# Kernel tuning notes

Hardware: AMD Instinct MI355X
Metric: run time of the kernel (lower is better)

The kernel has to match this reference:

```python
import jax, jax.numpy as jnp
import numpy as np

B, SI, ST, C, H, D = 1, 1024, 256, 3072, 24, 128
MLP = 4 * C
EPS = 1e-6
SCALE = 1.0 / float(np.sqrt(D))


def _ln(x):
    m = jnp.mean(x, -1, keepdims=True)
    v = jnp.var(x, -1, keepdims=True)
    return (x - m) / jnp.sqrt(v + EPS)


def _rms(x, w):
    return x * jax.lax.rsqrt(jnp.mean(x * x, -1, keepdims=True) + EPS) * w


def _mod(x, shift, scale):
    # AdaLN modulation: x * (1 + scale) + shift, scale/shift are [B, C]
    return x * (1.0 + scale[:, None, :]) + shift[:, None, :]


def _rot_half(x):
    xr, xi = x[..., 0::2], x[..., 1::2]
    return jnp.stack([-xi, xr], -1).reshape(x.shape)


def _rope(x, cos, sin):
    # x: [B, S, H, D]; cos/sin: [S, D]
    return x * cos[None, :, None, :] + _rot_half(x) * sin[None, :, None, :]


def _forward(img, txt, vec, fc, fs,
             i_mod_w, i_mod_b, i_qkv_w, i_qkv_b, i_qn, i_kn, i_pw, i_pb, i_f1w, i_f1b, i_f2w, i_f2b,
             t_mod_w, t_mod_b, t_qkv_w, t_qkv_b, t_qn, t_kn, t_pw, t_pb, t_f1w, t_f1b, t_f2w, t_f2b):
    sv = jax.nn.silu(vec)
    i_s1, i_c1, i_g1, i_s2, i_c2, i_g2 = jnp.split(sv @ i_mod_w + i_mod_b, 6, -1)
    t_s1, t_c1, t_g1, t_s2, t_c2, t_g2 = jnp.split(sv @ t_mod_w + t_mod_b, 6, -1)

    # img stream: LN -> modulate -> QKV -> qk RMSNorm -> RoPE
    iqkv = (_mod(_ln(img), i_s1, i_c1) @ i_qkv_w + i_qkv_b).reshape(B, SI, 3, H, D)
    iq = _rope(_rms(iqkv[:, :, 0], i_qn), fc, fs)
    ik = _rope(_rms(iqkv[:, :, 1], i_kn), fc, fs)
    iv = iqkv[:, :, 2]

    # txt stream: no RoPE
    tqkv = (_mod(_ln(txt), t_s1, t_c1) @ t_qkv_w + t_qkv_b).reshape(B, ST, 3, H, D)
    tq = _rms(tqkv[:, :, 0], t_qn)
    tk = _rms(tqkv[:, :, 1], t_kn)
    tv = tqkv[:, :, 2]

    q = jnp.concatenate([iq, tq], 1)
    k = jnp.concatenate([ik, tk], 1)
    v = jnp.concatenate([iv, tv], 1)

    logits = jnp.einsum('bqhd,bkhd->bhqk', q, k) * SCALE
    o = jnp.einsum('bhqk,bkhd->bqhd', jax.nn.softmax(logits, -1), v).reshape(B, SI + ST, C)
    ia, ta = o[:, :SI], o[:, SI:]

    img = img + (ia @ i_pw + i_pb) * i_g1[:, None, :]
    h = jax.nn.gelu(_mod(_ln(img), i_s2, i_c2) @ i_f1w + i_f1b, approximate=True)
    img = img + (h @ i_f2w + i_f2b) * i_g2[:, None, :]

    txt = txt + (ta @ t_pw + t_pb) * t_g1[:, None, :]
    h = jax.nn.gelu(_mod(_ln(txt), t_s2, t_c2) @ t_f1w + t_f1b, approximate=True)
    txt = txt + (h @ t_f2w + t_f2b) * t_g2[:, None, :]
    return img, txt


def setup_inputs() -> dict:
    key = jax.random.key(0)
    ki = iter(jax.random.split(key, 32))

    def w(shape, s=0.02):
        return jax.random.normal(next(ki), shape, jnp.float32) * s

    # RoPE tables shaped (img_seq_len, head_dim), interleaved pair layout
    pos = jnp.arange(SI, dtype=jnp.float32)
    inv = 1.0 / (10000.0 ** (jnp.arange(0, D, 2, dtype=jnp.float32) / D))
    ang = pos[:, None] * inv[None, :]
    inp = dict(
        img=jax.random.normal(next(ki), (B, SI, C), jnp.float32),
        txt=jax.random.normal(next(ki), (B, ST, C), jnp.float32),
        vec=jax.random.normal(next(ki), (B, C), jnp.float32),
        freqs_cos=jnp.repeat(jnp.cos(ang), 2, -1),
        freqs_sin=jnp.repeat(jnp.sin(ang), 2, -1),
    )
    for p in ('i', 't'):
        inp[p + '_mod_w'] = w((C, 6 * C)); inp[p + '_mod_b'] = jnp.zeros((6 * C,), jnp.float32)
        inp[p + '_qkv_w'] = w((C, 3 * C)); inp[p + '_qkv_b'] = jnp.zeros((3 * C,), jnp.float32)
        inp[p + '_qn'] = jnp.ones((D,), jnp.float32); inp[p + '_kn'] = jnp.ones((D,), jnp.float32)
        inp[p + '_pw'] = w((C, C)); inp[p + '_pb'] = jnp.zeros((C,), jnp.float32)
        inp[p + '_f1w'] = w((C, MLP)); inp[p + '_f1b'] = jnp.zeros((MLP,), jnp.float32)
        inp[p + '_f2w'] = w((MLP, C)); inp[p + '_f2b'] = jnp.zeros((C,), jnp.float32)
    return inp


def reference(img, txt, vec, freqs_cos, freqs_sin,
              i_mod_w, i_mod_b, i_qkv_w, i_qkv_b, i_qn, i_kn, i_pw, i_pb, i_f1w, i_f1b, i_f2w, i_f2b,
              t_mod_w, t_mod_b, t_qkv_w, t_qkv_b, t_qn, t_kn, t_pw, t_pb, t_f1w, t_f1b, t_f2w, t_f2b):
    return _forward(img, txt, vec, freqs_cos, freqs_sin,
                    i_mod_w, i_mod_b, i_qkv_w, i_qkv_b, i_qn, i_kn, i_pw, i_pb, i_f1w, i_f1b, i_f2w, i_f2b,
                    t_mod_w, t_mod_b, t_qkv_w, t_qkv_b, t_qn, t_kn, t_pw, t_pb, t_f1w, t_f1b, t_f2w, t_f2b)
```

## Files before the change

kernel.cpp:

```cpp
#include <hip/hip_runtime.h>


#define SI 1024
#define ST 256
#define SS 1280
#define CC 3072
#define NH 24
#define DH 128
#define MLPD 12288
#define EPSF 1e-6f
#define SCALEF 0.08838834764831845f

typedef __attribute__((ext_vector_type(4))) float f32x4;
typedef __attribute__((ext_vector_type(8))) __bf16 bf16x8;
typedef unsigned short u16;
typedef unsigned int u32;

__device__ __forceinline__ u16 f2bf(float x) {
    union { float f; u32 u; } v; v.f = x;
    u32 r = v.u + 0x7FFFu + ((v.u >> 16) & 1u);
    return (u16)(r >> 16);
}

__device__ __forceinline__ int gsw(int r) {
    return ((r >> 2) & 7) ^ ((r & 3) << 1);
}

__global__ __launch_bounds__(256) void k_modvec(
    const float* __restrict__ vec,
    const float* __restrict__ wi, const float* __restrict__ bi,
    const float* __restrict__ wt, const float* __restrict__ bt,
    float* __restrict__ mi, float* __restrict__ mt)
{
    __shared__ float sv[CC];
    __shared__ float part[7][128];
    int t = threadIdx.x;
    for (int i = t; i < CC; i += 256) {
        float x = vec[i];
        sv[i] = x / (1.f + __expf(-x));
    }
    __syncthreads();
    int gc = blockIdx.x;
    int strm = gc >= 144;
    const float* W  = strm ? wt : wi;
    const float* Bv = strm ? bt : bi;
    float* out      = strm ? mt : mi;
    int c0 = (gc % 144) * 128 + 4 * (t & 31);
    int g  = t >> 5;
    const float* wp  = W + (size_t)(g * 384) * (6 * CC) + c0;
    const float* svp = sv + g * 384;
    f32x4 acc = {0.f, 0.f, 0.f, 0.f};
    for (int r = 0; r < 384; ++r) {
        f32x4 wr = *(const f32x4*)(wp + (size_t)r * (6 * CC));
        float s = svp[r];
        acc.x += wr.x * s; acc.y += wr.y * s; acc.z += wr.z * s; acc.w += wr.w * s;
    }
    int li = t & 31;
    if (g > 0) *(f32x4*)&part[g - 1][li * 4] = acc;
    __syncthreads();
    if (g == 0) {
#pragma unroll
        for (int i = 0; i < 7; ++i) {
            f32x4 p = *(const f32x4*)&part[i][li * 4];
            acc.x += p.x; acc.y += p.y; acc.z += p.z; acc.w += p.w;
        }
        f32x4 bb = *(const f32x4*)(Bv + c0);
        acc.x += bb.x; acc.y += bb.y; acc.z += bb.z; acc.w += bb.w;
        *(f32x4*)(out + c0) = acc;
    }
}

__global__ __launch_bounds__(256) void k_lnmod(
    const float* __restrict__ x,
    const float* __restrict__ shift, const float* __restrict__ scale,
    u16* __restrict__ out)
{
    int r = blockIdx.x;
    const float* xp = x + (size_t)r * CC;
    u16* op = out + (size_t)r * CC;
    int t = threadIdx.x;
    float4 v[3];
    float s = 0.f, q = 0.f;
#pragma unroll
    for (int j = 0; j < 3; ++j) {
        v[j] = *(const float4*)(xp + j * 1024 + t * 4);
        s += v[j].x + v[j].y + v[j].z + v[j].w;
        q += v[j].x * v[j].x + v[j].y * v[j].y + v[j].z * v[j].z + v[j].w * v[j].w;
    }
#pragma unroll
    for (int m = 32; m; m >>= 1) { s += __shfl_xor(s, m); q += __shfl_xor(q, m); }
    __shared__ float red[8];
    int w = t >> 6;
    if ((t & 63) == 0) { red[w] = s; red[4 + w] = q; }
    __syncthreads();
    s = red[0] + red[1] + red[2] + red[3];
    q = red[4] + red[5] + red[6] + red[7];
    float mean = s * (1.f / CC);
    float var  = q * (1.f / CC) - mean * mean;
    float inv  = rsqrtf(var + EPSF);
#pragma unroll
    for (int j = 0; j < 3; ++j) {
        int c0 = j * 1024 + t * 4;
        float4 sh = *(const float4*)(shift + c0);
        float4 sc = *(const float4*)(scale + c0);
        ushort4 o;
        o.x = f2bf((v[j].x - mean) * inv * (1.f + sc.x) + sh.x);
        o.y = f2bf((v[j].y - mean) * inv * (1.f + sc.y) + sh.y);
        o.z = f2bf((v[j].z - mean) * inv * (1.f + sc.z) + sh.z);
        o.w = f2bf((v[j].w - mean) * inv * (1.f + sc.w) + sh.w);
        *(ushort4*)(op + c0) = o;
    }
}

template <int V, int BN>
__global__ __launch_bounds__(512, 2) void k_gemm(
    const u16* __restrict__ A,
    const float* __restrict__ Wi, const float* __restrict__ Wt,
    const float* __restrict__ bi, const float* __restrict__ bt,
    void* __restrict__ outv, int MBI, int N, int K, int lda)
{
    constexpr int BM  = 256;
    constexpr int NWN = (BN == 256) ? 4 : 2;
    constexpr int WM  = (BN == 256) ? 128 : 64;
    constexpr int MI  = WM / 16;
    constexpr int NFB = (BN == 256) ? 8 : 4;

    __shared__ u16 lA[2][BM * 64];
    __shared__ u16 lB[2][BN * 64];
    int t = threadIdx.x;
    int m0 = blockIdx.y * BM;
    int n0 = blockIdx.x * BN;
    bool txts = (blockIdx.y >= (unsigned)MBI);
    const float* W = txts ? Wt : Wi;
    const size_t koff = (size_t)blockIdx.z * K;

    int w = t >> 6, lane = t & 63;
    int wm = (w / NWN) * WM, wn = (w % NWN) * 64;
    int lr = lane & 15, lg = lane >> 4;

    f32x4 acc[MI][4];
#pragma unroll
    for (int i = 0; i < MI; ++i)
#pragma unroll
        for (int j = 0; j < 4; ++j) acc[i][j] = (f32x4){0.f, 0.f, 0.f, 0.f};

    const int bn4 = (BN == 256) ? 4 * (t & 63) : 4 * (t & 31);
    const int bk  = (BN == 256) ? 8 * (t >> 6) : 4 * (t >> 5);
    f32x4 fb[NFB];
    const int NT = K >> 6;

    auto LOADB = [&](int kt) {
        size_t kb = koff + (size_t)kt * 64 + bk;
#pragma unroll
        for (int i = 0; i < NFB; ++i)
            fb[i] = *(const f32x4*)(W + (kb + i) * (size_t)N + n0 + bn4);
    };
    auto GLDSA = [&](int kt, int buf) {
        size_t kb = koff + (size_t)kt * 64;
#pragma unroll
        for (int i = 0; i < 4; ++i) {
            int D = i * 512 + t; int row = D >> 3;
            int c = (D & 7) ^ gsw(row);
            const u16* gp = A + (size_t)(m0 + row) * lda + kb + c * 8;
            u16* lp = &lA[buf][D * 8];
            __builtin_amdgcn_global_load_lds(
                (const __attribute__((address_space(1))) void*)gp,
                (__attribute__((address_space(3))) void*)lp, 16, 0, 0);
        }
    };
    auto CVTWR = [&](int buf) {
        if constexpr (BN == 256) {
#pragma unroll
            for (int j = 0; j < 4; ++j) {
                int n = bn4 + j;
                union { uint4 q; __bf16 h[8]; } u;
#pragma unroll
                for (int i = 0; i < 8; ++i) u.h[i] = (__bf16)fb[i][j];
                int cp = (bk >> 3) ^ gsw(n);
                *(uint4*)&lB[buf][n * 64 + cp * 8] = u.q;
            }
        } else {
#pragma unroll
            for (int j = 0; j < 4; ++j) {
                int n = bn4 + j;
                union { uint2 q; __bf16 h[4]; } u;
#pragma unroll
                for (int i = 0; i < 4; ++i) u.h[i] = (__bf16)fb[i][j];
                int cp = (bk >> 3) ^ gsw(n);
                *(uint2*)&lB[buf][n * 64 + cp * 8 + (bk & 4)] = u.q;
            }
        }
    };
    auto MFMAP = [&](int buf) {
#pragma unroll
        for (int ks = 0; ks < 2; ++ks) {
            bf16x8 bv[4];
#pragma unroll
            for (int j = 0; j < 4; ++j) {
                int n = wn + j * 16 + lr;
                bv[j] = *(const bf16x8*)&lB[buf][n * 64 + (((ks * 4 + lg) ^ gsw(n)) * 8)];
            }
#pragma unroll
            for (int mh = 0; mh < MI / 4; ++mh) {
                bf16x8 af[4];
#pragma unroll
                for (int i2 = 0; i2 < 4; ++i2) {
                    int m = wm + (mh * 4 + i2) * 16 + lr;
                    af[i2] = *(const bf16x8*)&lA[buf][m * 64 + (((ks * 4 + lg) ^ gsw(m)) * 8)];
                }
                __builtin_amdgcn_s_setprio(1);
#pragma unroll
                for (int i2 = 0; i2 < 4; ++i2)
#pragma unroll
                    for (int j = 0; j < 4; ++j)
                        acc[mh * 4 + i2][j] = __builtin_amdgcn_mfma_f32_16x16x32_bf16(
                            af[i2], bv[j], acc[mh * 4 + i2][j], 0, 0, 0);
                __builtin_amdgcn_s_setprio(0);
            }
        }
    };
    auto VMWN = [&]() {
        if constexpr (BN == 256)
            asm volatile("s_waitcnt vmcnt(8) lgkmcnt(0)" ::: "memory");
        else
            asm volatile("s_waitcnt vmcnt(4) lgkmcnt(0)" ::: "memory");
    };

    LOADB(0);
    GLDSA(0, 0);
    CVTWR(0);
    if (NT > 1) LOADB(1);
    VMWN();
    __builtin_amdgcn_s_barrier();
    __builtin_amdgcn_sched_barrier(0);

    int cur = 0;
    for (int kt = 0; kt < NT; ++kt) {
        bool s1 = kt + 1 < NT;
        bool s2 = kt + 2 < NT;
        if (s1) {
            GLDSA(kt + 1, cur ^ 1);
            CVTWR(cur ^ 1);
        }
        if (s2) LOADB(kt + 2);
        MFMAP(cur);
        if (s1) {
            if (s2) { VMWN(); }
            else    { asm volatile("s_waitcnt vmcnt(0) lgkmcnt(0)" ::: "memory"); }
            __builtin_amdgcn_s_barrier();
            __builtin_amdgcn_sched_barrier(0);
        }
        cur ^= 1;
    }

    const float* Bb = txts ? bt : bi;
    int MT = gridDim.y * BM;
#pragma unroll
    for (int i = 0; i < MI; ++i) {
#pragma unroll
        for (int j = 0; j < 4; ++j) {
            int col = n0 + wn + j * 16 + lr;
            float bvv = (V == 3) ? 0.f : Bb[col];
#pragma unroll
            for (int e = 0; e < 4; ++e) {
                int row = m0 + wm + i * 16 + lg * 4 + e;
                float val = acc[i][j][e] + bvv;
                if (V == 0) {
                    ((float*)outv)[(size_t)row * N + col] = val;
                } else if (V == 1) {
                    float g = 0.5f * val * (1.f + tanhf(0.7978845608028654f * (val + 0.044715f * val * val * val)));
                    ((u16*)outv)[(size_t)row * N + col] = f2bf(g);
                } else {
                    ((float*)outv)[((size_t)blockIdx.z * MT + row) * N + col] = val;
                }
            }
        }
    }
}

__global__ __launch_bounds__(256) void k_red(
    const float* __restrict__ p,
    const float* __restrict__ bi, const float* __restrict__ bt,
    const float* __restrict__ gi, const float* __restrict__ gt,
    const float* __restrict__ basei, const float* __restrict__ baset,
    float* __restrict__ out)
{
    int idx4 = blockIdx.x * 256 + threadIdx.x;
    size_t idx = (size_t)idx4 * 4;
    const size_t MN = (size_t)SS * CC;
    int r = idx4 / 768;
    int c = (idx4 - r * 768) * 4;
    bool ts = r >= SI;
    float4 v0 = *(const float4*)(p + idx);
    float4 v1 = *(const float4*)(p + MN + idx);
    float4 bb = *(const float4*)((ts ? bt : bi) + c);
    float4 gg = *(const float4*)((ts ? gt : gi) + c);
    const float* bp = ts ? (baset + (size_t)(r - SI) * CC + c) : (basei + (size_t)r * CC + c);
    float4 ba = *(const float4*)bp;
    float4 o;
    o.x = ba.x + (v0.x + v1.x + bb.x) * gg.x;
    o.y = ba.y + (v0.y + v1.y + bb.y) * gg.y;
    o.z = ba.z + (v0.z + v1.z + bb.z) * gg.z;
    o.w = ba.w + (v0.w + v1.w + bb.w) * gg.w;
    *(float4*)(out + idx) = o;
}

__global__ __launch_bounds__(256) void k_pack(
    const float* __restrict__ qkv,
    const float* __restrict__ iqn, const float* __restrict__ ikn,
    const float* __restrict__ tqn, const float* __restrict__ tkn,
    const float* __restrict__ fc, const float* __restrict__ fs,
    u16* __restrict__ qpk, u16* __restrict__ kpk, u16* __restrict__ vpk)
{
    int wid = blockIdx.x * 4 + (threadIdx.x >> 6);
    int lane = threadIdx.x & 63;
    int s = wid / 72;
    int wh = wid % 72;
    int which = wh / 24;
    int h = wh % 24;
    int d = lane * 2;
    const float* src = qkv + (size_t)s * 9216 + which * 3072 + h * 128 + d;
    float x0 = src[0], x1 = src[1];
    float y0 = x0, y1 = x1;
    if (which < 2) {
        float ssq = x0 * x0 + x1 * x1;
#pragma unroll
        for (int m = 32; m; m >>= 1) ssq += __shfl_xor(ssq, m);
        float inv = rsqrtf(ssq * (1.f / 128.f) + EPSF);
        bool isimg = (s < SI);
        const float* wv = (which == 0) ? (isimg ? iqn : tqn) : (isimg ? ikn : tkn);
        y0 = x0 * inv * wv[d];
        y1 = x1 * inv * wv[d + 1];
        if (isimg) {
            float c0 = fc[s * 128 + d], c1 = fc[s * 128 + d + 1];
            float s0 = fs[s * 128 + d], s1 = fs[s * 128 + d + 1];
            float r0 = y0 * c0 - y1 * s0;
            float r1 = y1 * c1 + y0 * s1;
            y0 = r0; y1 = r1;
        }
        if (which == 0) { y0 *= SCALEF; y1 *= SCALEF; }
    }
    u16* dst = (which == 0) ? qpk : (which == 1) ? kpk : vpk;
    ushort2 o; o.x = f2bf(y0); o.y = f2bf(y1);
    *(ushort2*)(dst + ((size_t)h * SS + s) * 128 + d) = o;
}

__global__ __launch_bounds__(256, 1) void k_attn(
    const u16* __restrict__ qpk, const u16* __restrict__ kpk,
    const u16* __restrict__ vpk, u16* __restrict__ o)
{
    __shared__ u16 lK[128 * 136];
    __shared__ u16 lV[128 * 136];
    __shared__ u16 lP[128 * 136];
    int h = blockIdx.y;
    int q0 = blockIdx.x * 128;
    int t = threadIdx.x, w = t >> 6, lane = t & 63;
    int lr = lane & 15, lg = lane >> 4;
    const u16* qh = qpk + (size_t)h * SS * 128;
    const u16* kh = kpk + (size_t)h * SS * 128;
    const u16* vh = vpk + (size_t)h * SS * 128;

    bf16x8 aq[2][4];
#pragma unroll
    for (int mi = 0; mi < 2; ++mi)
#pragma unroll
        for (int kk = 0; kk < 4; ++kk)
            aq[mi][kk] = *(const bf16x8*)(qh + (size_t)(q0 + w * 32 + mi * 16 + lr) * 128 + kk * 32 + lg * 8);

    const f32x4 fz = {0.f, 0.f, 0.f, 0.f};
    f32x4 oa[2][8];
#pragma unroll
    for (int i = 0; i < 2; ++i)
#pragma unroll
        for (int j = 0; j < 8; ++j) oa[i][j] = fz;
    float mrow[2][4], lrow[2][4];
#pragma unroll
    for (int i = 0; i < 2; ++i)
#pragma unroll
        for (int e = 0; e < 4; ++e) { mrow[i][e] = -1e30f; lrow[i][e] = 0.f; }

    for (int kt = 0; kt < 10; ++kt) {
        int t0 = kt * 128;
        __syncthreads();
#pragma unroll
        for (int it = 0; it < 8; ++it) {
            int c = it * 256 + t;
            int row = c >> 4, part = c & 15;
            uint4 d4 = *(const uint4*)(kh + (size_t)(t0 + row) * 128 + part * 8);
            *(uint4*)(&lK[row * 136 + part * 8]) = d4;
        }
#pragma unroll
        for (int it = 0; it < 8; ++it) {
            int c = it * 256 + t;
            int tt = c >> 4, d0 = (c & 15) * 8;
            uint4 d4 = *(const uint4*)(vh + (size_t)(t0 + tt) * 128 + d0);
            const u16* e8 = (const u16*)&d4;
#pragma unroll
            for (int j = 0; j < 8; ++j) lV[(d0 + j) * 136 + tt] = e8[j];
        }
        __syncthreads();
        f32x4 sa[2][8];
#pragma unroll
        for (int i = 0; i < 2; ++i)
#pragma unroll
            for (int j = 0; j < 8; ++j) sa[i][j] = fz;
#pragma unroll
        for (int kk = 0; kk < 4; ++kk) {
            bf16x8 bk[8];
#pragma unroll
            for (int ni = 0; ni < 8; ++ni)
                bk[ni] = *(const bf16x8*)(&lK[(ni * 16 + lr) * 136 + kk * 32 + lg * 8]);
#pragma unroll
            for (int mi = 0; mi < 2; ++mi)
#pragma unroll
                for (int ni = 0; ni < 8; ++ni)
                    sa[mi][ni] = __builtin_amdgcn_mfma_f32_16x16x32_bf16(aq[mi][kk], bk[ni], sa[mi][ni], 0, 0, 0);
        }
#pragma unroll
        for (int mi = 0; mi < 2; ++mi) {
#pragma unroll
            for (int e = 0; e < 4; ++e) {
                float mx = sa[mi][0][e];
#pragma unroll
                for (int ni = 1; ni < 8; ++ni) mx = fmaxf(mx, sa[mi][ni][e]);
#pragma unroll
                for (int msk = 1; msk < 16; msk <<= 1) mx = fmaxf(mx, __shfl_xor(mx, msk));
                float mnew = fmaxf(mrow[mi][e], mx);
                float esc = __expf(mrow[mi][e] - mnew);
                mrow[mi][e] = mnew;
                float rsum = 0.f;
#pragma unroll
                for (int ni = 0; ni < 8; ++ni) {
                    float p = __expf(sa[mi][ni][e] - mnew);
                    sa[mi][ni][e] = p;
                    rsum += p;
                }
#pragma unroll
                for (int msk = 1; msk < 16; msk <<= 1) rsum += __shfl_xor(rsum, msk);
                lrow[mi][e] = lrow[mi][e] * esc + rsum;
#pragma unroll
                for (int nd = 0; nd < 8; ++nd) oa[mi][nd][e] *= esc;
            }
        }
#pragma unroll
        for (int mi = 0; mi < 2; ++mi)
#pragma unroll
            for (int ni = 0; ni < 8; ++ni)
#pragma unroll
                for (int e = 0; e < 4; ++e)
                    lP[(w * 32 + mi * 16 + lg * 4 + e) * 136 + ni * 16 + lr] = f2bf(sa[mi][ni][e]);
        __syncthreads();
#pragma unroll
        for (int kk = 0; kk < 4; ++kk) {
            bf16x8 pa[2], vb[8];
#pragma unroll
            for (int mi = 0; mi < 2; ++mi)
                pa[mi] = *(const bf16x8*)(&lP[(w * 32 + mi * 16 + lr) * 136 + kk * 32 + lg * 8]);
#pragma unroll
            for (int nd = 0; nd < 8; ++nd)
                vb[nd] = *(const bf16x8*)(&lV[(nd * 16 + lr) * 136 + kk * 32 + lg * 8]);
#pragma unroll
            for (int mi = 0; mi < 2; ++mi)
#pragma unroll
                for (int nd = 0; nd < 8; ++nd)
                    oa[mi][nd] = __builtin_amdgcn_mfma_f32_16x16x32_bf16(pa[mi], vb[nd], oa[mi][nd], 0, 0, 0);
        }
    }
#pragma unroll
    for (int mi = 0; mi < 2; ++mi) {
#pragma unroll
        for (int nd = 0; nd < 8; ++nd) {
#pragma unroll
            for (int e = 0; e < 4; ++e) {
                int row = q0 + w * 32 + mi * 16 + lg * 4 + e;
                int col = h * 128 + nd * 16 + lr;
                o[(size_t)row * CC + col] = f2bf(oa[mi][nd][e] / lrow[mi][e]);
            }
        }
    }
}

extern "C" void kernel_launch(void* const* d_in, const int* in_sizes, int n_in,
                              void* d_out, int out_size, void* d_ws, size_t ws_size,
                              hipStream_t stream)
{
    const float* img  = (const float*)d_in[0];
    const float* txt  = (const float*)d_in[1];
    const float* vec  = (const float*)d_in[2];
    const float* fc   = (const float*)d_in[3];
    const float* fs   = (const float*)d_in[4];
    const float* i_mod_w = (const float*)d_in[5];
    const float* i_mod_b = (const float*)d_in[6];
    const float* i_qkv_w = (const float*)d_in[7];
    const float* i_qkv_b = (const float*)d_in[8];
    const float* i_qn  = (const float*)d_in[9];
    const float* i_kn  = (const float*)d_in[10];
    const float* i_pw  = (const float*)d_in[11];
    const float* i_pb  = (const float*)d_in[12];
    const float* i_f1w = (const float*)d_in[13];
    const float* i_f1b = (const float*)d_in[14];
    const float* i_f2w = (const float*)d_in[15];
    const float* i_f2b = (const float*)d_in[16];
    const float* t_mod_w = (const float*)d_in[17];
    const float* t_mod_b = (const float*)d_in[18];
    const float* t_qkv_w = (const float*)d_in[19];
    const float* t_qkv_b = (const float*)d_in[20];
    const float* t_qn  = (const float*)d_in[21];
    const float* t_kn  = (const float*)d_in[22];
    const float* t_pw  = (const float*)d_in[23];
    const float* t_pb  = (const float*)d_in[24];
    const float* t_f1w = (const float*)d_in[25];
    const float* t_f1b = (const float*)d_in[26];
    const float* t_f2w = (const float*)d_in[27];
    const float* t_f2b = (const float*)d_in[28];

    char* ws = (char*)d_ws;
    float* mod_i = (float*)(ws + 0);
    float* mod_t = (float*)(ws + 73728);
    u16*   xmod  = (u16*)(ws + 147456);
    float* qkv   = (float*)(ws + 8011776);
    u16*   qpk   = (u16*)(ws + 55197696);
    u16*   kpk   = (u16*)(ws + 63062016);
    u16*   vpk   = (u16*)(ws + 70926336);
    u16*   obuf  = (u16*)(ws + 78790656);
    u16*   hbuf  = (u16*)(ws + 8011776);
    float* pbufP = (float*)(ws + 8011776);
    float* pbufF = (float*)(ws + 39469056);

    float* out_img = (float*)d_out;
    float* out_txt = out_img + (size_t)SI * CC;

    k_modvec<<<288, 256, 0, stream>>>(vec, i_mod_w, i_mod_b, t_mod_w, t_mod_b, mod_i, mod_t);

    k_lnmod<<<SI, 256, 0, stream>>>(img, mod_i + 0, mod_i + 3072, xmod);
    k_lnmod<<<ST, 256, 0, stream>>>(txt, mod_t + 0, mod_t + 3072, xmod + (size_t)SI * CC);

    k_gemm<0, 256><<<dim3(36, 5, 1), 512, 0, stream>>>(xmod, i_qkv_w, t_qkv_w, i_qkv_b, t_qkv_b,
                                                       qkv, 4, 9216, CC, CC);

    k_pack<<<23040, 256, 0, stream>>>(qkv, i_qn, i_kn, t_qn, t_kn, fc, fs, qpk, kpk, vpk);

    k_attn<<<dim3(10, 24), 256, 0, stream>>>(qpk, kpk, vpk, obuf);

    k_gemm<3, 128><<<dim3(24, 5, 2), 512, 0, stream>>>(obuf, i_pw, t_pw, nullptr, nullptr,
                                                       pbufP, 4, CC, CC / 2, CC);
    k_red<<<3840, 256, 0, stream>>>(pbufP, i_pb, t_pb, mod_i + 6144, mod_t + 6144,
                                    img, txt, out_img);

    k_lnmod<<<SI, 256, 0, stream>>>(out_img, mod_i + 9216, mod_i + 12288, xmod);
    k_lnmod<<<ST, 256, 0, stream>>>(out_txt, mod_t + 9216, mod_t + 12288, xmod + (size_t)SI * CC);

    k_gemm<1, 256><<<dim3(48, 5, 1), 512, 0, stream>>>(xmod, i_f1w, t_f1w, i_f1b, t_f1b,
                                                       hbuf, 4, MLPD, CC, CC);

    k_gemm<3, 128><<<dim3(24, 5, 2), 512, 0, stream>>>(hbuf, i_f2w, t_f2w, nullptr, nullptr,
                                                       pbufF, 4, CC, MLPD / 2, MLPD);
    k_red<<<3840, 256, 0, stream>>>(pbufF, i_f2b, t_f2b, mod_i + 15360, mod_t + 15360,
                                    out_img, out_txt, out_img);
}
```

Baseline: 720.2 us.

## Unroll GEMM k-loop by two and widen attention to 512 threads

The GEMM main loop is unrolled by two so LDS buffer indices are compile-time constants, which removes the cur toggle and the per-iteration branches; this assumes NT is even. The attention kernel moves from 4 to 8 waves per block, each owning 16 query rows, which halves per-wave register use and adds parallelism. The V transpose into LDS now packs two tokens per 32-bit store and uses an XOR swizzle to cut bank conflicts. The __syncthreads between writing and reading P is dropped, which is safe only because each wave reads back just its own P rows.

```diff
diff --git a/kernel.cpp b/kernel.cpp
--- a/kernel.cpp
+++ b/kernel.cpp
@@ -225,32 +225,38 @@
         else
             asm volatile("s_waitcnt vmcnt(4) lgkmcnt(0)" ::: "memory");
     };
+    auto VMW0 = [&]() {
+        asm volatile("s_waitcnt vmcnt(0) lgkmcnt(0)" ::: "memory");
+    };
 
     LOADB(0);
     GLDSA(0, 0);
     CVTWR(0);
-    if (NT > 1) LOADB(1);
+    LOADB(1);
     VMWN();
     __builtin_amdgcn_s_barrier();
     __builtin_amdgcn_sched_barrier(0);
 
-    int cur = 0;
-    for (int kt = 0; kt < NT; ++kt) {
-        bool s1 = kt + 1 < NT;
-        bool s2 = kt + 2 < NT;
-        if (s1) {
-            GLDSA(kt + 1, cur ^ 1);
-            CVTWR(cur ^ 1);
-        }
-        if (s2) LOADB(kt + 2);
-        MFMAP(cur);
-        if (s1) {
-            if (s2) { VMWN(); }
-            else    { asm volatile("s_waitcnt vmcnt(0) lgkmcnt(0)" ::: "memory"); }
+    for (int kt = 0; kt < NT; kt += 2) {
+        bool more = kt + 2 < NT;
+        GLDSA(kt + 1, 1);
+        CVTWR(1);
+        if (more) LOADB(kt + 2);
+        MFMAP(0);
+        if (more) VMWN(); else VMW0();
+        __builtin_amdgcn_s_barrier();
+        __builtin_amdgcn_sched_barrier(0);
+        if (more) {
+            GLDSA(kt + 2, 0);
+            CVTWR(0);
+            LOADB(kt + 3);
+        }
+        MFMAP(1);
+        if (more) {
+            VMWN();
             __builtin_amdgcn_s_barrier();
             __builtin_amdgcn_sched_barrier(0);
         }
-        cur ^= 1;
     }
 
     const float* Bb = txts ? bt : bi;
@@ -345,7 +351,7 @@
     *(ushort2*)(dst + ((size_t)h * SS + s) * 128 + d) = o;
 }
 
-__global__ __launch_bounds__(256, 1) void k_attn(
+__global__ __launch_bounds__(512, 1) void k_attn(
     const u16* __restrict__ qpk, const u16* __restrict__ kpk,
     const u16* __restrict__ vpk, u16* __restrict__ o)
 {
@@ -360,50 +366,51 @@
     const u16* kh = kpk + (size_t)h * SS * 128;
     const u16* vh = vpk + (size_t)h * SS * 128;
 
-    bf16x8 aq[2][4];
-#pragma unroll
-    for (int mi = 0; mi < 2; ++mi)
-#pragma unroll
-        for (int kk = 0; kk < 4; ++kk)
-            aq[mi][kk] = *(const bf16x8*)(qh + (size_t)(q0 + w * 32 + mi * 16 + lr) * 128 + kk * 32 + lg * 8);
+    bf16x8 aq[4];
+#pragma unroll
+    for (int kk = 0; kk < 4; ++kk)
+        aq[kk] = *(const bf16x8*)(qh + (size_t)(q0 + w * 16 + lr) * 128 + kk * 32 + lg * 8);
 
     const f32x4 fz = {0.f, 0.f, 0.f, 0.f};
-    f32x4 oa[2][8];
-#pragma unroll
-    for (int i = 0; i < 2; ++i)
-#pragma unroll
-        for (int j = 0; j < 8; ++j) oa[i][j] = fz;
-    float mrow[2][4], lrow[2][4];
-#pragma unroll
-    for (int i = 0; i < 2; ++i)
-#pragma unroll
-        for (int e = 0; e < 4; ++e) { mrow[i][e] = -1e30f; lrow[i][e] = 0.f; }
+    f32x4 oa[8];
+#pragma unroll
+    for (int j = 0; j < 8; ++j) oa[j] = fz;
+    float mrow[4], lrow[4];
+#pragma unroll
+    for (int e = 0; e < 4; ++e) { mrow[e] = -1e30f; lrow[e] = 0.f; }
 
     for (int kt = 0; kt < 10; ++kt) {
         int t0 = kt * 128;
         __syncthreads();
 #pragma unroll
-        for (int it = 0; it < 8; ++it) {
-            int c = it * 256 + t;
+        for (int it = 0; it < 4; ++it) {
+            int c = it * 512 + t;
             int row = c >> 4, part = c & 15;
             uint4 d4 = *(const uint4*)(kh + (size_t)(t0 + row) * 128 + part * 8);
             *(uint4*)(&lK[row * 136 + part * 8]) = d4;
         }
 #pragma unroll
-        for (int it = 0; it < 8; ++it) {
-            int c = it * 256 + t;
-            int tt = c >> 4, d0 = (c & 15) * 8;
-            uint4 d4 = *(const uint4*)(vh + (size_t)(t0 + tt) * 128 + d0);
-            const u16* e8 = (const u16*)&d4;
-#pragma unroll
-            for (int j = 0; j < 8; ++j) lV[(d0 + j) * 136 + tt] = e8[j];
+        for (int it = 0; it < 2; ++it) {
+            int c = it * 512 + t;
+            int pr = c >> 4;
+            int tt = pr * 2;
+            int k = c & 15;
+            int d0 = k * 8;
+            uint4 a = *(const uint4*)(vh + (size_t)(t0 + tt) * 128 + d0);
+            uint4 b = *(const uint4*)(vh + (size_t)(t0 + tt + 1) * 128 + d0);
+            const u16* a16 = (const u16*)&a;
+            const u16* b16 = (const u16*)&b;
+            int ts = tt ^ ((k & 7) << 3);
+#pragma unroll
+            for (int j = 0; j < 8; ++j) {
+                ushort2 pv; pv.x = a16[j]; pv.y = b16[j];
+                *(ushort2*)(&lV[(d0 + j) * 136 + ts]) = pv;
+            }
         }
         __syncthreads();
-        f32x4 sa[2][8];
-#pragma unroll
-        for (int i = 0; i < 2; ++i)
-#pragma unroll
-            for (int j = 0; j < 8; ++j) sa[i][j] = fz;
+        f32x4 sa[8];
+#pragma unroll
+        for (int j = 0; j < 8; ++j) sa[j] = fz;
 #pragma unroll
         for (int kk = 0; kk < 4; ++kk) {
             bf16x8 bk[8];
@@ -411,71 +418,59 @@
             for (int ni = 0; ni < 8; ++ni)
                 bk[ni] = *(const bf16x8*)(&lK[(ni * 16 + lr) * 136 + kk * 32 + lg * 8]);
 #pragma unroll
-            for (int mi = 0; mi < 2; ++mi)
-#pragma unroll
-                for (int ni = 0; ni < 8; ++ni)
-                    sa[mi][ni] = __builtin_amdgcn_mfma_f32_16x16x32_bf16(aq[mi][kk], bk[ni], sa[mi][ni], 0, 0, 0);
-        }
-#pragma unroll
-        for (int mi = 0; mi < 2; ++mi) {
-#pragma unroll
-            for (int e = 0; e < 4; ++e) {
-                float mx = sa[mi][0][e];
-#pragma unroll
-                for (int ni = 1; ni < 8; ++ni) mx = fmaxf(mx, sa[mi][ni][e]);
-#pragma unroll
-                for (int msk = 1; msk < 16; msk <<= 1) mx = fmaxf(mx, __shfl_xor(mx, msk));
-                float mnew = fmaxf(mrow[mi][e], mx);
-                float esc = __expf(mrow[mi][e] - mnew);
-                mrow[mi][e] = mnew;
-                float rsum = 0.f;
-#pragma unroll
-                for (int ni = 0; ni < 8; ++ni) {
-                    float p = __expf(sa[mi][ni][e] - mnew);
-                    sa[mi][ni][e] = p;
-                    rsum += p;
-                }
-#pragma unroll
-                for (int msk = 1; msk < 16; msk <<= 1) rsum += __shfl_xor(rsum, msk);
-                lrow[mi][e] = lrow[mi][e] * esc + rsum;
-#pragma unroll
-                for (int nd = 0; nd < 8; ++nd) oa[mi][nd][e] *= esc;
-            }
-        }
-#pragma unroll
-        for (int mi = 0; mi < 2; ++mi)
-#pragma unroll
             for (int ni = 0; ni < 8; ++ni)
-#pragma unroll
-                for (int e = 0; e < 4; ++e)
-                    lP[(w * 32 + mi * 16 + lg * 4 + e) * 136 + ni * 16 + lr] = f2bf(sa[mi][ni][e]);
-        __syncthreads();
+                sa[ni] = __builtin_amdgcn_mfma_f32_16x16x32_bf16(aq[kk], bk[ni], sa[ni], 0, 0, 0);
+        }
+#pragma unroll
+        for (int e = 0; e < 4; ++e) {
+            float mx = sa[0][e];
+#pragma unroll
+            for (int ni = 1; ni < 8; ++ni) mx = fmaxf(mx, sa[ni][e]);
+#pragma unroll
+            for (int msk = 1; msk < 16; msk <<= 1) mx = fmaxf(mx, __shfl_xor(mx, msk));
+            float mnew = fmaxf(mrow[e], mx);
+            float esc = __expf(mrow[e] - mnew);
+            mrow[e] = mnew;
+            float rsum = 0.f;
+#pragma unroll
+            for (int ni = 0; ni < 8; ++ni) {
+                float p = __expf(sa[ni][e] - mnew);
+                sa[ni][e] = p;
+                rsum += p;
+            }
+#pragma unroll
+            for (int msk = 1; msk < 16; msk <<= 1) rsum += __shfl_xor(rsum, msk);
+            lrow[e] = lrow[e] * esc + rsum;
+#pragma unroll
+            for (int nd = 0; nd < 8; ++nd) oa[nd][e] *= esc;
+        }
+#pragma unroll
+        for (int ni = 0; ni < 8; ++ni)
+#pragma unroll
+            for (int e = 0; e < 4; ++e)
+                lP[(w * 16 + lg * 4 + e) * 136 + ni * 16 + lr] = f2bf(sa[ni][e]);
 #pragma unroll
         for (int kk = 0; kk < 4; ++kk) {
-            bf16x8 pa[2], vb[8];
-#pragma unroll
-            for (int mi = 0; mi < 2; ++mi)
-                pa[mi] = *(const bf16x8*)(&lP[(w * 32 + mi * 16 + lr) * 136 + kk * 32 + lg * 8]);
+            bf16x8 pa, vb[8];
+            pa = *(const bf16x8*)(&lP[(w * 16 + lr) * 136 + kk * 32 + lg * 8]);
+#pragma unroll
+            for (int nd = 0; nd < 8; ++nd) {
+                int d = nd * 16 + lr;
+                int ch = (kk * 4 + lg) ^ ((d >> 3) & 7);
+                vb[nd] = *(const bf16x8*)(&lV[d * 136 + ch * 8]);
+            }
 #pragma unroll
             for (int nd = 0; nd < 8; ++nd)
-                vb[nd] = *(const bf16x8*)(&lV[(nd * 16 + lr) * 136 + kk * 32 + lg * 8]);
-#pragma unroll
-            for (int mi = 0; mi < 2; ++mi)
-#pragma unroll
-                for (int nd = 0; nd < 8; ++nd)
-                    oa[mi][nd] = __builtin_amdgcn_mfma_f32_16x16x32_bf16(pa[mi], vb[nd], oa[mi][nd], 0, 0, 0);
-        }
-    }
-#pragma unroll
-    for (int mi = 0; mi < 2; ++mi) {
-#pragma unroll
-        for (int nd = 0; nd < 8; ++nd) {
-#pragma unroll
-            for (int e = 0; e < 4; ++e) {
-                int row = q0 + w * 32 + mi * 16 + lg * 4 + e;
-                int col = h * 128 + nd * 16 + lr;
-                o[(size_t)row * CC + col] = f2bf(oa[mi][nd][e] / lrow[mi][e]);
-            }
+                oa[nd] = __builtin_amdgcn_mfma_f32_16x16x32_bf16(pa, vb[nd], oa[nd], 0, 0, 0);
+        }
+    }
+#pragma unroll
+    for (int nd = 0; nd < 8; ++nd) {
+#pragma unroll
+        for (int e = 0; e < 4; ++e) {
+            int row = q0 + w * 16 + lg * 4 + e;
+            int col = h * 128 + nd * 16 + lr;
+            o[(size_t)row * CC + col] = f2bf(oa[nd][e] / lrow[e]);
         }
     }
 }
@@ -540,7 +535,7 @@
 
     k_pack<<<23040, 256, 0, stream>>>(qkv, i_qn, i_kn, t_qn, t_kn, fc, fs, qpk, kpk, vpk);
 
-    k_attn<<<dim3(10, 24), 256, 0, stream>>>(qpk, kpk, vpk, obuf);
+    k_attn<<<dim3(10, 24), 512, 0, stream>>>(qpk, kpk, vpk, obuf);
 
     k_gemm<3, 128><<<dim3(24, 5, 2), 512, 0, stream>>>(obuf, i_pw, t_pw, nullptr, nullptr,
                                                        pbufP, 4, CC, CC / 2, CC);
```

Measured after the change: 1.575 ms. 119% more time.
